# Kernel tuning notes

Measured on AMD Instinct MI355X. Metric: run time of the kernel, lower is better.

The kernel has to match this reference:

```python
import jax, jax.numpy as jnp
import numpy as np

B_SZ, L, H, P = 16, 1024, 256, 256
DT_MIN, DT_MAX = 1e-3, 1e-1


def setup_inputs() -> dict:
    key = jax.random.key(0)
    ks = jax.random.split(key, 6)
    u = jax.random.normal(ks[0], (B_SZ, L, H), dtype=jnp.float32)
    # Stable diagonal init (stands in for HiPPO-LegS diag: negative real part,
    # spread imaginary parts) so exp(Lambda*Delta) has |.|<1 over long scans.
    Lambda_re = -0.5 * jnp.ones((P,), jnp.float32)
    Lambda_im = jnp.pi * jnp.arange(P, dtype=jnp.float32)
    Bp = jax.random.normal(ks[1], (P, H, 2), jnp.float32) / jnp.sqrt(2.0 * H)  # (P,H,2) real/imag
    Cp = jax.random.normal(ks[2], (H, P, 2), jnp.float32) / jnp.sqrt(2.0 * P)  # (H,P,2) real/imag
    D = jax.random.normal(ks[3], (H,), jnp.float32)
    log_step = (jax.random.uniform(ks[4], (P, 1), jnp.float32)
                * (jnp.log(DT_MAX) - jnp.log(DT_MIN)) + jnp.log(DT_MIN))
    return {"u": u, "Lambda_re": Lambda_re, "Lambda_im": Lambda_im,
            "B": Bp, "C": Cp, "D": D, "log_step": log_step}


def _binop(ei, ej):
    # S5 associative scan element: (A, Bu); compose linear recurrences.
    ai, bi = ei
    aj, bj = ej
    return aj * ai, aj * bi + bj


def reference(u, Lambda_re, Lambda_im, B, C, D, log_step):
    # clip_eigs=False, step_rescale=1.0, conj_sym=True, discretization='zoh'
    Lambda = Lambda_re + 1j * Lambda_im                     # (P,) complex
    B_tilde = B[..., 0] + 1j * B[..., 1]                    # (P,H) complex
    C_tilde = C[..., 0] + 1j * C[..., 1]                    # (H,P) complex
    Delta = jnp.exp(log_step[:, 0])                         # (P,)
    # ZOH discretization
    Lambda_bar = jnp.exp(Lambda * Delta)                    # (P,)
    B_bar = ((Lambda_bar - 1.0) / Lambda)[:, None] * B_tilde  # (P,H)
    # Input projection: (B, L, P) complex
    Bu = jnp.einsum('ph,blh->blp', B_bar, u.astype(B_bar.dtype))
    Lam = jnp.broadcast_to(Lambda_bar, Bu.shape)            # (B, L, P)
    # Parallel associative scan over time axis
    _, xs = jax.lax.associative_scan(_binop, (Lam, Bu), axis=1)  # states (B,L,P)
    # Output projection; conj_sym -> 2 * real part
    ys = 2.0 * jnp.einsum('hp,blp->blh', C_tilde, xs).real  # (B,L,H)
    return ys + D * u                                       # feedthrough
```

## Files before the change

### kernel.cpp

```cpp
#include <hip/hip_runtime.h>
#include <hip/hip_bf16.h>
#include <math.h>

#define BB     16
#define LSEQ   1024
#define HH     256
#define PP     256
#define MROWS  (BB*LSEQ)
#define LC     32
#define NC     (LSEQ/LC)
#define NCHUNK (BB*NC)

#define OFF_W1T  0u
#define OFF_W2T  262144u
#define OFF_CEND 524288u
#define OFF_CPRE 1572864u
#define OFF_XS   2621440u

typedef __attribute__((ext_vector_type(8))) short short8;
typedef __attribute__((ext_vector_type(4))) float floatx4;

__device__ __forceinline__ float bf2f(unsigned hs) {
    union { unsigned u; float f; } v; v.u = hs << 16; return v.f;
}
__device__ __forceinline__ unsigned short f2bs(float f) {
    __hip_bfloat16 h = __float2bfloat16(f);
    union { __hip_bfloat16 h; unsigned short s; } v; v.h = h; return v.s;
}
__device__ __forceinline__ unsigned packbf(float r, float i) {
    return (unsigned)f2bs(r) | ((unsigned)f2bs(i) << 16);
}
__device__ __forceinline__ void async16(const void* g, void* l) {
    __builtin_amdgcn_global_load_lds(
        (const __attribute__((address_space(1))) unsigned*)g,
        (__attribute__((address_space(3))) unsigned*)l, 16, 0, 0);
}
__device__ __forceinline__ float2 lam_pow(float lr, float li, float dtt) {
    float m = expf(lr * dtt);
    return make_float2(m * cosf(li * dtt), m * sinf(li * dtt));
}

__global__ void k_prep(const float* __restrict__ Bm, const float* __restrict__ Cm,
                       const float* __restrict__ Lr, const float* __restrict__ Li,
                       const float* __restrict__ ls, char* __restrict__ ws) {
    int blk = blockIdx.x, t = threadIdx.x;
    if (blk < 256) {
        int p = blk, h = t;
        float lr = Lr[p], li = Li[p];
        float dt = expf(ls[p]);
        float2 lam = lam_pow(lr, li, dt);
        float den = lr * lr + li * li;
        float nr = lam.x - 1.0f, ni = lam.y;
        float cr = (nr * lr + ni * li) / den;
        float ci = (ni * lr - nr * li) / den;
        float br = Bm[(p * HH + h) * 2 + 0];
        float bi = Bm[(p * HH + h) * 2 + 1];
        unsigned short* w1 = (unsigned short*)(ws + OFF_W1T);
        w1[(2 * p) * 256 + h]     = f2bs(cr * br - ci * bi);
        w1[(2 * p + 1) * 256 + h] = f2bs(cr * bi + ci * br);
    } else {
        int h = blk - 256, p = t;
        float c_r = Cm[(h * PP + p) * 2 + 0];
        float c_i = Cm[(h * PP + p) * 2 + 1];
        ((unsigned*)(ws + OFF_W2T))[h * 256 + p] = packbf(2.0f * c_r, -2.0f * c_i);
    }
}

__global__ __launch_bounds__(256) void k_g1scan(
        const float* __restrict__ u, const float* __restrict__ Lr,
        const float* __restrict__ Li, const float* __restrict__ ls,
        char* __restrict__ ws) {
    __shared__ char smem[2048 + 32768];
    unsigned short* As = (unsigned short*)smem;
    char* Bs = smem + 2048;
    const unsigned short* W = (const unsigned short*)(ws + OFF_W1T);
    const int tid = threadIdx.x;
    const int wave = tid >> 6, lane = tid & 63;
    const int q = lane >> 4, rr = lane & 15;
    const int c4 = lane & 3, r4 = lane >> 2;
    const int bc = blockIdx.x;
    const int m0 = bc * LC;

    floatx4 acc[2][8];
    #pragma unroll
    for (int i = 0; i < 2; ++i)
        #pragma unroll
        for (int j = 0; j < 8; ++j) acc[i][j] = (floatx4)0.0f;

    const int urow = tid >> 3, ucol4 = (tid & 7) * 4;
    for (int k0 = 0; k0 < 256; k0 += 32) {
        __syncthreads();
        float4 v = *(const float4*)(u + (size_t)(m0 + urow) * 256 + k0 + ucol4);
        *(uint2*)((char*)As + urow * 64 + ucol4 * 2) =
            make_uint2(packbf(v.x, v.y), packbf(v.z, v.w));
        #pragma unroll
        for (int t = wave; t < 32; t += 4)
            async16(W + (size_t)(t * 16 + r4) * 256 + k0 + c4 * 8,
                    Bs + t * 1024 + lane * 16);
        __syncthreads();
        short8 a0 = *(const short8*)((char*)As + rr * 64 + q * 16);
        short8 a1 = *(const short8*)((char*)As + (16 + rr) * 64 + q * 16);
        #pragma unroll
        for (int j = 0; j < 8; ++j) {
            short8 b = *(const short8*)(Bs + ((wave * 8 + j) * 16 + rr) * 64 + q * 16);
            acc[0][j] = __builtin_amdgcn_mfma_f32_16x16x32_bf16(a0, b, acc[0][j], 0, 0, 0);
            acc[1][j] = __builtin_amdgcn_mfma_f32_16x16x32_bf16(a1, b, acc[1][j], 0, 0, 0);
        }
    }

    __syncthreads();
    unsigned short* X = (unsigned short*)Bs;
    #pragma unroll
    for (int i = 0; i < 2; ++i)
        #pragma unroll
        for (int j = 0; j < 8; ++j)
            #pragma unroll
            for (int r0 = 0; r0 < 4; ++r0)
                X[(i * 16 + q * 4 + r0) * 512 + wave * 128 + j * 16 + rr] =
                    f2bs(acc[i][j][r0]);
    __syncthreads();

    int p = tid;
    float dt = expf(ls[p]);
    float2 lam = lam_pow(Lr[p], Li[p], dt);
    unsigned* X32 = (unsigned*)Bs;
    unsigned* xs32 = (unsigned*)(ws + OFF_XS);
    float xr = 0.0f, xi = 0.0f;
    for (int j = 0; j < LC; ++j) {
        unsigned cv = X32[j * 256 + p];
        float br = bf2f(cv & 0xffffu), bi = bf2f(cv >> 16);
        float nr = fmaf(lam.x, xr, fmaf(-lam.y, xi, br));
        float ni = fmaf(lam.x, xi, fmaf(lam.y, xr, bi));
        xr = nr; xi = ni;
        xs32[(size_t)(m0 + j) * 256 + p] = packbf(xr, xi);
    }
    ((float2*)(ws + OFF_CEND))[bc * 256 + p] = make_float2(xr, xi);
}

__global__ void k_scanB(const float* __restrict__ Lr, const float* __restrict__ Li,
                        const float* __restrict__ ls, char* __restrict__ ws) {
    int p = threadIdx.x, b = blockIdx.x;
    float dt = expf(ls[p]);
    float2 g = lam_pow(Lr[p], Li[p], dt * LC);
    float2* cend = (float2*)(ws + OFF_CEND);
    float2* cpre = (float2*)(ws + OFF_CPRE);
    float sr = 0.0f, si = 0.0f;
    for (int c = 0; c < NC; ++c) {
        int off = (b * NC + c) * 256 + p;
        cpre[off] = make_float2(sr, si);
        float2 e = cend[off];
        float nr = g.x * sr - g.y * si + e.x;
        float ni = g.x * si + g.y * sr + e.y;
        sr = nr; si = ni;
    }
}

__global__ void k_scanC(const float* __restrict__ Lr, const float* __restrict__ Li,
                        const float* __restrict__ ls, char* __restrict__ ws) {
    int p = threadIdx.x, bc = blockIdx.x;
    float dt = expf(ls[p]);
    float2 lam = lam_pow(Lr[p], Li[p], dt);
    float2 cr = ((const float2*)(ws + OFF_CPRE))[bc * 256 + p];
    float pr = lam.x, pi = lam.y;
    unsigned* xs32 = (unsigned*)(ws + OFF_XS);
    size_t idx = (size_t)bc * LC * 256 + p;
    for (int j = 0; j < LC; ++j) {
        float ar = pr * cr.x - pi * cr.y;
        float ai = pr * cr.y + pi * cr.x;
        unsigned v = xs32[idx];
        xs32[idx] = packbf(bf2f(v & 0xffffu) + ar, bf2f(v >> 16) + ai);
        float nr = pr * lam.x - pi * lam.y;
        pi = pr * lam.y + pi * lam.x; pr = nr;
        idx += 256;
    }
}

__global__ __launch_bounds__(256) void k_gemm2(
        const char* __restrict__ ws_c, const float* __restrict__ D,
        const float* __restrict__ u, float* __restrict__ out) {
    __shared__ unsigned short As[128 * 32];
    __shared__ unsigned short Bs[128 * 32];
    const unsigned short* A = (const unsigned short*)(ws_c + OFF_XS);
    const unsigned short* W = (const unsigned short*)(ws_c + OFF_W2T);
    const int tid = threadIdx.x;
    const int wave = tid >> 6, lane = tid & 63;
    const int q = lane >> 4, rr = lane & 15;
    const int c4 = lane & 3, r4 = lane >> 2;
    const int wm = wave & 1, wn = wave >> 1;
    const int m0 = blockIdx.y * 128, n0 = blockIdx.x * 128;

    floatx4 acc[4][4];
    #pragma unroll
    for (int i = 0; i < 4; ++i)
        #pragma unroll
        for (int j = 0; j < 4; ++j) acc[i][j] = (floatx4)0.0f;

    for (int k0 = 0; k0 < 512; k0 += 32) {
        __syncthreads();
        #pragma unroll
        for (int t = wave; t < 8; t += 4)
            async16(A + (size_t)(m0 + t * 16 + r4) * 512 + k0 + c4 * 8,
                    (char*)As + t * 1024 + lane * 16);
        #pragma unroll
        for (int t = wave; t < 8; t += 4)
            async16(W + (size_t)(n0 + t * 16 + r4) * 512 + k0 + c4 * 8,
                    (char*)Bs + t * 1024 + lane * 16);
        __syncthreads();
        short8 a[4], b[4];
        #pragma unroll
        for (int i = 0; i < 4; ++i)
            a[i] = *(const short8*)((const char*)As + (wm * 64 + i * 16 + rr) * 64 + q * 16);
        #pragma unroll
        for (int j = 0; j < 4; ++j)
            b[j] = *(const short8*)((const char*)Bs + (wn * 64 + j * 16 + rr) * 64 + q * 16);
        #pragma unroll
        for (int i = 0; i < 4; ++i)
            #pragma unroll
            for (int j = 0; j < 4; ++j)
                acc[i][j] = __builtin_amdgcn_mfma_f32_16x16x32_bf16(a[i], b[j], acc[i][j], 0, 0, 0);
    }

    #pragma unroll
    for (int i = 0; i < 4; ++i) {
        int mbase = m0 + wm * 64 + i * 16 + q * 4;
        #pragma unroll
        for (int j = 0; j < 4; ++j) {
            int col = n0 + wn * 64 + j * 16 + rr;
            #pragma unroll
            for (int r0 = 0; r0 < 4; ++r0) {
                int row = mbase + r0;
                float v = acc[i][j][r0] + D[col] * u[(size_t)row * 256 + col];
                out[(size_t)row * 256 + col] = v;
            }
        }
    }
}

extern "C" void kernel_launch(void* const* d_in, const int* in_sizes, int n_in,
                              void* d_out, int out_size, void* d_ws, size_t ws_size,
                              hipStream_t stream) {
    const float* u  = (const float*)d_in[0];
    const float* Lr = (const float*)d_in[1];
    const float* Li = (const float*)d_in[2];
    const float* Bm = (const float*)d_in[3];
    const float* Cm = (const float*)d_in[4];
    const float* D  = (const float*)d_in[5];
    const float* ls = (const float*)d_in[6];
    float* out = (float*)d_out;
    char* ws = (char*)d_ws;

    k_prep<<<512, 256, 0, stream>>>(Bm, Cm, Lr, Li, ls, ws);
    k_g1scan<<<NCHUNK, 256, 0, stream>>>(u, Lr, Li, ls, ws);
    k_scanB<<<BB, 256, 0, stream>>>(Lr, Li, ls, ws);
    k_scanC<<<NCHUNK, 256, 0, stream>>>(Lr, Li, ls, ws);
    k_gemm2<<<dim3(2, MROWS / 128), 256, 0, stream>>>(ws, D, u, out);
}
```

Measured before the change: 123.4 us.

## Fuse prep, chunk scan, carry propagation and output GEMM into one cooperative kernel

Replaces five kernel launches with a single cooperative kernel that uses grid-wide syncs between the weight prep, the chunked input GEMM and scan, and the carry fix-up plus output GEMM. Each block keeps its 32-row chunk of scan states in padded shared memory, so the xs tensor never goes through global memory. Each block recomputes its own chunk carry prefix serially from the chunk-end states instead of running a separate scan kernel. In exchange it depends on all 512 blocks being co-resident, pays for grid barriers, and uses about 51 KB of LDS per block, which can lower occupancy.

```diff
diff --git a/kernel.cpp b/kernel.cpp
--- a/kernel.cpp
+++ b/kernel.cpp
@@ -1,12 +1,14 @@
 #include <hip/hip_runtime.h>
 #include <hip/hip_bf16.h>
+#include <hip/hip_cooperative_groups.h>
 #include <math.h>
+
+namespace cg = cooperative_groups;
 
 #define BB     16
 #define LSEQ   1024
 #define HH     256
 #define PP     256
-#define MROWS  (BB*LSEQ)
 #define LC     32
 #define NC     (LSEQ/LC)
 #define NCHUNK (BB*NC)
@@ -14,8 +16,8 @@
 #define OFF_W1T  0u
 #define OFF_W2T  262144u
 #define OFF_CEND 524288u
-#define OFF_CPRE 1572864u
-#define OFF_XS   2621440u
+
+#define XSTRIDE 520
 
 typedef __attribute__((ext_vector_type(8))) short short8;
 typedef __attribute__((ext_vector_type(4))) float floatx4;
@@ -40,62 +42,64 @@
     return make_float2(m * cosf(li * dtt), m * sinf(li * dtt));
 }
 
-__global__ void k_prep(const float* __restrict__ Bm, const float* __restrict__ Cm,
-                       const float* __restrict__ Lr, const float* __restrict__ Li,
-                       const float* __restrict__ ls, char* __restrict__ ws) {
-    int blk = blockIdx.x, t = threadIdx.x;
-    if (blk < 256) {
-        int p = blk, h = t;
-        float lr = Lr[p], li = Li[p];
-        float dt = expf(ls[p]);
-        float2 lam = lam_pow(lr, li, dt);
-        float den = lr * lr + li * li;
-        float nr = lam.x - 1.0f, ni = lam.y;
-        float cr = (nr * lr + ni * li) / den;
-        float ci = (ni * lr - nr * li) / den;
+__global__ __launch_bounds__(256, 2) void k_fused(
+        const float* __restrict__ u, const float* __restrict__ Lr,
+        const float* __restrict__ Li, const float* __restrict__ Bm,
+        const float* __restrict__ Cm, const float* __restrict__ D,
+        const float* __restrict__ ls, float* __restrict__ out,
+        char* __restrict__ ws) {
+    cg::grid_group grid = cg::this_grid();
+    __shared__ char smem[51712];
+    unsigned short* As = (unsigned short*)smem;
+    char*           Bs = smem + 2048;
+    unsigned short* X  = (unsigned short*)(smem + 2048);
+    unsigned*      X32 = (unsigned*)(smem + 2048);
+    char*          Bs2 = smem + 35328;
+
+    const int tid = threadIdx.x, bc = blockIdx.x;
+    const int wave = tid >> 6, lane = tid & 63;
+    const int q = lane >> 4, rr = lane & 15;
+    const int c4 = lane & 3, r4 = lane >> 2;
+
+    if (bc < 256) {
+        int p = bc, h = tid;
+        float lr0 = Lr[p], li0 = Li[p];
+        float dt0 = expf(ls[p]);
+        float2 lam0 = lam_pow(lr0, li0, dt0);
+        float den = lr0 * lr0 + li0 * li0;
+        float nr = lam0.x - 1.0f, ni = lam0.y;
+        float cr = (nr * lr0 + ni * li0) / den;
+        float ci = (ni * lr0 - nr * li0) / den;
         float br = Bm[(p * HH + h) * 2 + 0];
         float bi = Bm[(p * HH + h) * 2 + 1];
         unsigned short* w1 = (unsigned short*)(ws + OFF_W1T);
         w1[(2 * p) * 256 + h]     = f2bs(cr * br - ci * bi);
         w1[(2 * p + 1) * 256 + h] = f2bs(cr * bi + ci * br);
     } else {
-        int h = blk - 256, p = t;
+        int h = bc - 256, p = tid;
         float c_r = Cm[(h * PP + p) * 2 + 0];
         float c_i = Cm[(h * PP + p) * 2 + 1];
         ((unsigned*)(ws + OFF_W2T))[h * 256 + p] = packbf(2.0f * c_r, -2.0f * c_i);
     }
-}
-
-__global__ __launch_bounds__(256) void k_g1scan(
-        const float* __restrict__ u, const float* __restrict__ Lr,
-        const float* __restrict__ Li, const float* __restrict__ ls,
-        char* __restrict__ ws) {
-    __shared__ char smem[2048 + 32768];
-    unsigned short* As = (unsigned short*)smem;
-    char* Bs = smem + 2048;
-    const unsigned short* W = (const unsigned short*)(ws + OFF_W1T);
-    const int tid = threadIdx.x;
-    const int wave = tid >> 6, lane = tid & 63;
-    const int q = lane >> 4, rr = lane & 15;
-    const int c4 = lane & 3, r4 = lane >> 2;
-    const int bc = blockIdx.x;
+    grid.sync();
+
     const int m0 = bc * LC;
-
+    const unsigned short* W1 = (const unsigned short*)(ws + OFF_W1T);
     floatx4 acc[2][8];
     #pragma unroll
     for (int i = 0; i < 2; ++i)
         #pragma unroll
         for (int j = 0; j < 8; ++j) acc[i][j] = (floatx4)0.0f;
 
-    const int urow = tid >> 3, ucol4 = (tid & 7) * 4;
+    const int urow = tid >> 3, ucol = (tid & 7) * 4;
     for (int k0 = 0; k0 < 256; k0 += 32) {
         __syncthreads();
-        float4 v = *(const float4*)(u + (size_t)(m0 + urow) * 256 + k0 + ucol4);
-        *(uint2*)((char*)As + urow * 64 + ucol4 * 2) =
+        float4 v = *(const float4*)(u + (size_t)(m0 + urow) * 256 + k0 + ucol);
+        *(uint2*)((char*)As + urow * 64 + ucol * 2) =
             make_uint2(packbf(v.x, v.y), packbf(v.z, v.w));
         #pragma unroll
         for (int t = wave; t < 32; t += 4)
-            async16(W + (size_t)(t * 16 + r4) * 256 + k0 + c4 * 8,
+            async16(W1 + (size_t)(t * 16 + r4) * 256 + k0 + c4 * 8,
                     Bs + t * 1024 + lane * 16);
         __syncthreads();
         short8 a0 = *(const short8*)((char*)As + rr * 64 + q * 16);
@@ -107,130 +111,91 @@
             acc[1][j] = __builtin_amdgcn_mfma_f32_16x16x32_bf16(a1, b, acc[1][j], 0, 0, 0);
         }
     }
-
     __syncthreads();
-    unsigned short* X = (unsigned short*)Bs;
     #pragma unroll
     for (int i = 0; i < 2; ++i)
         #pragma unroll
         for (int j = 0; j < 8; ++j)
             #pragma unroll
             for (int r0 = 0; r0 < 4; ++r0)
-                X[(i * 16 + q * 4 + r0) * 512 + wave * 128 + j * 16 + rr] =
+                X[(i * 16 + q * 4 + r0) * XSTRIDE + wave * 128 + j * 16 + rr] =
                     f2bs(acc[i][j][r0]);
     __syncthreads();
 
-    int p = tid;
-    float dt = expf(ls[p]);
-    float2 lam = lam_pow(Lr[p], Li[p], dt);
-    unsigned* X32 = (unsigned*)Bs;
-    unsigned* xs32 = (unsigned*)(ws + OFF_XS);
+    const int p = tid;
+    const float lr = Lr[p], li = Li[p];
+    const float dt = expf(ls[p]);
+    const float2 lam = lam_pow(lr, li, dt);
     float xr = 0.0f, xi = 0.0f;
     for (int j = 0; j < LC; ++j) {
-        unsigned cv = X32[j * 256 + p];
+        unsigned cv = X32[j * (XSTRIDE / 2) + p];
         float br = bf2f(cv & 0xffffu), bi = bf2f(cv >> 16);
         float nr = fmaf(lam.x, xr, fmaf(-lam.y, xi, br));
         float ni = fmaf(lam.x, xi, fmaf(lam.y, xr, bi));
         xr = nr; xi = ni;
-        xs32[(size_t)(m0 + j) * 256 + p] = packbf(xr, xi);
+        X32[j * (XSTRIDE / 2) + p] = packbf(xr, xi);
     }
     ((float2*)(ws + OFF_CEND))[bc * 256 + p] = make_float2(xr, xi);
-}
-
-__global__ void k_scanB(const float* __restrict__ Lr, const float* __restrict__ Li,
-                        const float* __restrict__ ls, char* __restrict__ ws) {
-    int p = threadIdx.x, b = blockIdx.x;
-    float dt = expf(ls[p]);
-    float2 g = lam_pow(Lr[p], Li[p], dt * LC);
-    float2* cend = (float2*)(ws + OFF_CEND);
-    float2* cpre = (float2*)(ws + OFF_CPRE);
+
+    grid.sync();
+
+    const int b = bc >> 5, c = bc & (NC - 1);
+    const float2 g = lam_pow(lr, li, dt * (float)LC);
+    const float2* cend = (const float2*)(ws + OFF_CEND);
     float sr = 0.0f, si = 0.0f;
-    for (int c = 0; c < NC; ++c) {
-        int off = (b * NC + c) * 256 + p;
-        cpre[off] = make_float2(sr, si);
-        float2 e = cend[off];
+    for (int cc = 0; cc < c; ++cc) {
+        float2 e = cend[(b * NC + cc) * 256 + p];
         float nr = g.x * sr - g.y * si + e.x;
         float ni = g.x * si + g.y * sr + e.y;
         sr = nr; si = ni;
     }
-}
-
-__global__ void k_scanC(const float* __restrict__ Lr, const float* __restrict__ Li,
-                        const float* __restrict__ ls, char* __restrict__ ws) {
-    int p = threadIdx.x, bc = blockIdx.x;
-    float dt = expf(ls[p]);
-    float2 lam = lam_pow(Lr[p], Li[p], dt);
-    float2 cr = ((const float2*)(ws + OFF_CPRE))[bc * 256 + p];
+
     float pr = lam.x, pi = lam.y;
-    unsigned* xs32 = (unsigned*)(ws + OFF_XS);
-    size_t idx = (size_t)bc * LC * 256 + p;
     for (int j = 0; j < LC; ++j) {
-        float ar = pr * cr.x - pi * cr.y;
-        float ai = pr * cr.y + pi * cr.x;
-        unsigned v = xs32[idx];
-        xs32[idx] = packbf(bf2f(v & 0xffffu) + ar, bf2f(v >> 16) + ai);
+        float ar = pr * sr - pi * si;
+        float ai = pr * si + pi * sr;
+        unsigned v = X32[j * (XSTRIDE / 2) + p];
+        X32[j * (XSTRIDE / 2) + p] = packbf(bf2f(v & 0xffffu) + ar,
+                                            bf2f(v >> 16) + ai);
         float nr = pr * lam.x - pi * lam.y;
         pi = pr * lam.y + pi * lam.x; pr = nr;
-        idx += 256;
-    }
-}
-
-__global__ __launch_bounds__(256) void k_gemm2(
-        const char* __restrict__ ws_c, const float* __restrict__ D,
-        const float* __restrict__ u, float* __restrict__ out) {
-    __shared__ unsigned short As[128 * 32];
-    __shared__ unsigned short Bs[128 * 32];
-    const unsigned short* A = (const unsigned short*)(ws_c + OFF_XS);
-    const unsigned short* W = (const unsigned short*)(ws_c + OFF_W2T);
-    const int tid = threadIdx.x;
-    const int wave = tid >> 6, lane = tid & 63;
-    const int q = lane >> 4, rr = lane & 15;
-    const int c4 = lane & 3, r4 = lane >> 2;
-    const int wm = wave & 1, wn = wave >> 1;
-    const int m0 = blockIdx.y * 128, n0 = blockIdx.x * 128;
-
-    floatx4 acc[4][4];
-    #pragma unroll
-    for (int i = 0; i < 4; ++i)
-        #pragma unroll
-        for (int j = 0; j < 4; ++j) acc[i][j] = (floatx4)0.0f;
+    }
+    __syncthreads();
+
+    const unsigned short* W2 = (const unsigned short*)(ws + OFF_W2T);
+    floatx4 acc2[2][4];
+    #pragma unroll
+    for (int i = 0; i < 2; ++i)
+        #pragma unroll
+        for (int j = 0; j < 4; ++j) acc2[i][j] = (floatx4)0.0f;
 
     for (int k0 = 0; k0 < 512; k0 += 32) {
         __syncthreads();
         #pragma unroll
-        for (int t = wave; t < 8; t += 4)
-            async16(A + (size_t)(m0 + t * 16 + r4) * 512 + k0 + c4 * 8,
-                    (char*)As + t * 1024 + lane * 16);
-        #pragma unroll
-        for (int t = wave; t < 8; t += 4)
-            async16(W + (size_t)(n0 + t * 16 + r4) * 512 + k0 + c4 * 8,
-                    (char*)Bs + t * 1024 + lane * 16);
-        __syncthreads();
-        short8 a[4], b[4];
-        #pragma unroll
-        for (int i = 0; i < 4; ++i)
-            a[i] = *(const short8*)((const char*)As + (wm * 64 + i * 16 + rr) * 64 + q * 16);
-        #pragma unroll
-        for (int j = 0; j < 4; ++j)
-            b[j] = *(const short8*)((const char*)Bs + (wn * 64 + j * 16 + rr) * 64 + q * 16);
-        #pragma unroll
-        for (int i = 0; i < 4; ++i)
-            #pragma unroll
-            for (int j = 0; j < 4; ++j)
-                acc[i][j] = __builtin_amdgcn_mfma_f32_16x16x32_bf16(a[i], b[j], acc[i][j], 0, 0, 0);
-    }
-
-    #pragma unroll
-    for (int i = 0; i < 4; ++i) {
-        int mbase = m0 + wm * 64 + i * 16 + q * 4;
+        for (int t = wave; t < 16; t += 4)
+            async16(W2 + (size_t)(t * 16 + r4) * 512 + k0 + c4 * 8,
+                    Bs2 + t * 1024 + lane * 16);
+        __syncthreads();
+        short8 a0 = *(const short8*)((char*)X + rr * (XSTRIDE * 2) + k0 * 2 + q * 16);
+        short8 a1 = *(const short8*)((char*)X + (16 + rr) * (XSTRIDE * 2) + k0 * 2 + q * 16);
         #pragma unroll
         for (int j = 0; j < 4; ++j) {
-            int col = n0 + wn * 64 + j * 16 + rr;
+            short8 bfr = *(const short8*)(Bs2 + ((wave * 4 + j) * 16 + rr) * 64 + q * 16);
+            acc2[0][j] = __builtin_amdgcn_mfma_f32_16x16x32_bf16(a0, bfr, acc2[0][j], 0, 0, 0);
+            acc2[1][j] = __builtin_amdgcn_mfma_f32_16x16x32_bf16(a1, bfr, acc2[1][j], 0, 0, 0);
+        }
+    }
+
+    #pragma unroll
+    for (int i = 0; i < 2; ++i) {
+        #pragma unroll
+        for (int j = 0; j < 4; ++j) {
+            int col = wave * 64 + j * 16 + rr;
             #pragma unroll
             for (int r0 = 0; r0 < 4; ++r0) {
-                int row = mbase + r0;
-                float v = acc[i][j][r0] + D[col] * u[(size_t)row * 256 + col];
-                out[(size_t)row * 256 + col] = v;
+                int row = m0 + i * 16 + q * 4 + r0;
+                size_t gi = (size_t)row * 256 + col;
+                out[gi] = acc2[i][j][r0] + D[col] * u[gi];
             }
         }
     }
@@ -249,9 +214,8 @@
     float* out = (float*)d_out;
     char* ws = (char*)d_ws;
 
-    k_prep<<<512, 256, 0, stream>>>(Bm, Cm, Lr, Li, ls, ws);
-    k_g1scan<<<NCHUNK, 256, 0, stream>>>(u, Lr, Li, ls, ws);
-    k_scanB<<<BB, 256, 0, stream>>>(Lr, Li, ls, ws);
-    k_scanC<<<NCHUNK, 256, 0, stream>>>(Lr, Li, ls, ws);
-    k_gemm2<<<dim3(2, MROWS / 128), 256, 0, stream>>>(ws, D, u, out);
-}
+    void* args[] = {(void*)&u, (void*)&Lr, (void*)&Li, (void*)&Bm, (void*)&Cm,
+                    (void*)&D, (void*)&ls, (void*)&out, (void*)&ws};
+    hipLaunchCooperativeKernel((const void*)k_fused, dim3(NCHUNK), dim3(256),
+                               args, 0, stream);
+}
```

Measured after the change: 229.7 us. 1.86x slower.

## Fuse chunk-carry scan into fixup kernel, widen g1scan blocks, shrink gemm2 tiles

Applied to the files above, without the earlier changes.

Replaces the serial per-batch carry scan (16 blocks) and the separate fixup kernel with a single kernel in which each chunk block recomputes its own incoming carry from earlier chunk ends. This removes a launch and the low-parallelism serial stage, at the cost of redundant work that grows quadratically with chunk index. The first GEMM+scan kernel now uses 512 threads, with only half of them running the scan, and pads its LDS row stride to reduce bank conflicts. The output GEMM uses 64x64 tiles so more blocks are launched for better occupancy.

```diff
diff --git a/kernel.cpp b/kernel.cpp
--- a/kernel.cpp
+++ b/kernel.cpp
@@ -14,8 +14,9 @@
 #define OFF_W1T  0u
 #define OFF_W2T  262144u
 #define OFF_CEND 524288u
-#define OFF_CPRE 1572864u
-#define OFF_XS   2621440u
+#define OFF_XS   1572864u
+
+#define XSTRIDE 520
 
 typedef __attribute__((ext_vector_type(8))) short short8;
 typedef __attribute__((ext_vector_type(4))) float floatx4;
@@ -66,107 +67,101 @@
     }
 }
 
-__global__ __launch_bounds__(256) void k_g1scan(
+__global__ __launch_bounds__(512, 4) void k_g1scan(
         const float* __restrict__ u, const float* __restrict__ Lr,
         const float* __restrict__ Li, const float* __restrict__ ls,
         char* __restrict__ ws) {
-    __shared__ char smem[2048 + 32768];
-    unsigned short* As = (unsigned short*)smem;
-    char* Bs = smem + 2048;
-    const unsigned short* W = (const unsigned short*)(ws + OFF_W1T);
-    const int tid = threadIdx.x;
+    __shared__ char smem[2048 + 33280];
+    unsigned*  As32 = (unsigned*)smem;
+    char*      Bs   = smem + 2048;
+    unsigned short* X = (unsigned short*)(smem + 2048);
+    unsigned*  X32  = (unsigned*)(smem + 2048);
+    const unsigned short* W1 = (const unsigned short*)(ws + OFF_W1T);
+    const int tid = threadIdx.x, bc = blockIdx.x;
     const int wave = tid >> 6, lane = tid & 63;
     const int q = lane >> 4, rr = lane & 15;
     const int c4 = lane & 3, r4 = lane >> 2;
-    const int bc = blockIdx.x;
     const int m0 = bc * LC;
 
-    floatx4 acc[2][8];
+    floatx4 acc[2][4];
     #pragma unroll
     for (int i = 0; i < 2; ++i)
         #pragma unroll
-        for (int j = 0; j < 8; ++j) acc[i][j] = (floatx4)0.0f;
-
-    const int urow = tid >> 3, ucol4 = (tid & 7) * 4;
+        for (int j = 0; j < 4; ++j) acc[i][j] = (floatx4)0.0f;
+
+    const int urow = tid >> 4, ucol2 = (tid & 15) * 2;
     for (int k0 = 0; k0 < 256; k0 += 32) {
         __syncthreads();
-        float4 v = *(const float4*)(u + (size_t)(m0 + urow) * 256 + k0 + ucol4);
-        *(uint2*)((char*)As + urow * 64 + ucol4 * 2) =
-            make_uint2(packbf(v.x, v.y), packbf(v.z, v.w));
-        #pragma unroll
-        for (int t = wave; t < 32; t += 4)
-            async16(W + (size_t)(t * 16 + r4) * 256 + k0 + c4 * 8,
+        float2 v = *(const float2*)(u + (size_t)(m0 + urow) * 256 + k0 + ucol2);
+        As32[urow * 16 + (tid & 15)] = packbf(v.x, v.y);
+        #pragma unroll
+        for (int t = wave; t < 32; t += 8)
+            async16(W1 + (size_t)(t * 16 + r4) * 256 + k0 + c4 * 8,
                     Bs + t * 1024 + lane * 16);
         __syncthreads();
-        short8 a0 = *(const short8*)((char*)As + rr * 64 + q * 16);
-        short8 a1 = *(const short8*)((char*)As + (16 + rr) * 64 + q * 16);
-        #pragma unroll
-        for (int j = 0; j < 8; ++j) {
-            short8 b = *(const short8*)(Bs + ((wave * 8 + j) * 16 + rr) * 64 + q * 16);
+        short8 a0 = *(const short8*)((char*)As32 + rr * 64 + q * 16);
+        short8 a1 = *(const short8*)((char*)As32 + (16 + rr) * 64 + q * 16);
+        #pragma unroll
+        for (int j = 0; j < 4; ++j) {
+            short8 b = *(const short8*)(Bs + ((wave * 4 + j) * 16 + rr) * 64 + q * 16);
             acc[0][j] = __builtin_amdgcn_mfma_f32_16x16x32_bf16(a0, b, acc[0][j], 0, 0, 0);
             acc[1][j] = __builtin_amdgcn_mfma_f32_16x16x32_bf16(a1, b, acc[1][j], 0, 0, 0);
         }
     }
-
     __syncthreads();
-    unsigned short* X = (unsigned short*)Bs;
     #pragma unroll
     for (int i = 0; i < 2; ++i)
         #pragma unroll
-        for (int j = 0; j < 8; ++j)
+        for (int j = 0; j < 4; ++j)
             #pragma unroll
             for (int r0 = 0; r0 < 4; ++r0)
-                X[(i * 16 + q * 4 + r0) * 512 + wave * 128 + j * 16 + rr] =
+                X[(i * 16 + q * 4 + r0) * XSTRIDE + wave * 64 + j * 16 + rr] =
                     f2bs(acc[i][j][r0]);
     __syncthreads();
 
-    int p = tid;
-    float dt = expf(ls[p]);
-    float2 lam = lam_pow(Lr[p], Li[p], dt);
-    unsigned* X32 = (unsigned*)Bs;
-    unsigned* xs32 = (unsigned*)(ws + OFF_XS);
-    float xr = 0.0f, xi = 0.0f;
-    for (int j = 0; j < LC; ++j) {
-        unsigned cv = X32[j * 256 + p];
-        float br = bf2f(cv & 0xffffu), bi = bf2f(cv >> 16);
-        float nr = fmaf(lam.x, xr, fmaf(-lam.y, xi, br));
-        float ni = fmaf(lam.x, xi, fmaf(lam.y, xr, bi));
-        xr = nr; xi = ni;
-        xs32[(size_t)(m0 + j) * 256 + p] = packbf(xr, xi);
-    }
-    ((float2*)(ws + OFF_CEND))[bc * 256 + p] = make_float2(xr, xi);
-}
-
-__global__ void k_scanB(const float* __restrict__ Lr, const float* __restrict__ Li,
-                        const float* __restrict__ ls, char* __restrict__ ws) {
-    int p = threadIdx.x, b = blockIdx.x;
-    float dt = expf(ls[p]);
-    float2 g = lam_pow(Lr[p], Li[p], dt * LC);
-    float2* cend = (float2*)(ws + OFF_CEND);
-    float2* cpre = (float2*)(ws + OFF_CPRE);
+    if (tid < 256) {
+        const int p = tid;
+        const float2 lam = lam_pow(Lr[p], Li[p], expf(ls[p]));
+        unsigned* xs32 = (unsigned*)(ws + OFF_XS);
+        float xr = 0.0f, xi = 0.0f;
+        for (int j = 0; j < LC; ++j) {
+            unsigned cv = X32[j * (XSTRIDE / 2) + p];
+            float br = bf2f(cv & 0xffffu), bi = bf2f(cv >> 16);
+            float nr = fmaf(lam.x, xr, fmaf(-lam.y, xi, br));
+            float ni = fmaf(lam.x, xi, fmaf(lam.y, xr, bi));
+            xr = nr; xi = ni;
+            xs32[(size_t)(m0 + j) * 256 + p] = packbf(xr, xi);
+        }
+        ((float2*)(ws + OFF_CEND))[bc * 256 + p] = make_float2(xr, xi);
+    }
+}
+
+__global__ __launch_bounds__(256) void k_scanBC(
+        const float* __restrict__ Lr, const float* __restrict__ Li,
+        const float* __restrict__ ls, char* __restrict__ ws) {
+    const int p = threadIdx.x, bc = blockIdx.x;
+    const int b = bc >> 5, c = bc & (NC - 1);
+    if (c == 0) return;
+    const float dt = expf(ls[p]);
+    const float lr = Lr[p], li = Li[p];
+    const float2 lam = lam_pow(lr, li, dt);
+    const float2 g = lam_pow(lr, li, dt * (float)LC);
+    const float2* cend = (const float2*)(ws + OFF_CEND);
+
     float sr = 0.0f, si = 0.0f;
-    for (int c = 0; c < NC; ++c) {
-        int off = (b * NC + c) * 256 + p;
-        cpre[off] = make_float2(sr, si);
-        float2 e = cend[off];
-        float nr = g.x * sr - g.y * si + e.x;
-        float ni = g.x * si + g.y * sr + e.y;
+    for (int cc = 0; cc < c; ++cc) {
+        float2 e = cend[(size_t)(b * NC + cc) * 256 + p];
+        float nr = fmaf(g.x, sr, fmaf(-g.y, si, e.x));
+        float ni = fmaf(g.x, si, fmaf(g.y, sr, e.y));
         sr = nr; si = ni;
     }
-}
-
-__global__ void k_scanC(const float* __restrict__ Lr, const float* __restrict__ Li,
-                        const float* __restrict__ ls, char* __restrict__ ws) {
-    int p = threadIdx.x, bc = blockIdx.x;
-    float dt = expf(ls[p]);
-    float2 lam = lam_pow(Lr[p], Li[p], dt);
-    float2 cr = ((const float2*)(ws + OFF_CPRE))[bc * 256 + p];
+
     float pr = lam.x, pi = lam.y;
     unsigned* xs32 = (unsigned*)(ws + OFF_XS);
     size_t idx = (size_t)bc * LC * 256 + p;
     for (int j = 0; j < LC; ++j) {
-        float ar = pr * cr.x - pi * cr.y;
-        float ai = pr * cr.y + pi * cr.x;
+        float ar = pr * sr - pi * si;
+        float ai = pr * si + pi * sr;
         unsigned v = xs32[idx];
         xs32[idx] = packbf(bf2f(v & 0xffffu) + ar, bf2f(v >> 16) + ai);
         float nr = pr * lam.x - pi * lam.y;
@@ -175,11 +170,11 @@
     }
 }
 
-__global__ __launch_bounds__(256) void k_gemm2(
+__global__ __launch_bounds__(256, 4) void k_gemm2(
         const char* __restrict__ ws_c, const float* __restrict__ D,
         const float* __restrict__ u, float* __restrict__ out) {
-    __shared__ unsigned short As[128 * 32];
-    __shared__ unsigned short Bs[128 * 32];
+    __shared__ unsigned short As[64 * 32];
+    __shared__ unsigned short Bs[64 * 32];
     const unsigned short* A = (const unsigned short*)(ws_c + OFF_XS);
     const unsigned short* W = (const unsigned short*)(ws_c + OFF_W2T);
     const int tid = threadIdx.x;
@@ -187,50 +182,46 @@
     const int q = lane >> 4, rr = lane & 15;
     const int c4 = lane & 3, r4 = lane >> 2;
     const int wm = wave & 1, wn = wave >> 1;
-    const int m0 = blockIdx.y * 128, n0 = blockIdx.x * 128;
-
-    floatx4 acc[4][4];
-    #pragma unroll
-    for (int i = 0; i < 4; ++i)
-        #pragma unroll
-        for (int j = 0; j < 4; ++j) acc[i][j] = (floatx4)0.0f;
+    const int m0 = blockIdx.y * 64, n0 = blockIdx.x * 64;
+
+    floatx4 acc[2][2];
+    #pragma unroll
+    for (int i = 0; i < 2; ++i)
+        #pragma unroll
+        for (int j = 0; j < 2; ++j) acc[i][j] = (floatx4)0.0f;
 
     for (int k0 = 0; k0 < 512; k0 += 32) {
         __syncthreads();
-        #pragma unroll
-        for (int t = wave; t < 8; t += 4)
-            async16(A + (size_t)(m0 + t * 16 + r4) * 512 + k0 + c4 * 8,
-                    (char*)As + t * 1024 + lane * 16);
-        #pragma unroll
-        for (int t = wave; t < 8; t += 4)
-            async16(W + (size_t)(n0 + t * 16 + r4) * 512 + k0 + c4 * 8,
-                    (char*)Bs + t * 1024 + lane * 16);
-        __syncthreads();
-        short8 a[4], b[4];
-        #pragma unroll
-        for (int i = 0; i < 4; ++i)
-            a[i] = *(const short8*)((const char*)As + (wm * 64 + i * 16 + rr) * 64 + q * 16);
-        #pragma unroll
-        for (int j = 0; j < 4; ++j)
-            b[j] = *(const short8*)((const char*)Bs + (wn * 64 + j * 16 + rr) * 64 + q * 16);
-        #pragma unroll
-        for (int i = 0; i < 4; ++i)
+        async16(A + (size_t)(m0 + wave * 16 + r4) * 512 + k0 + c4 * 8,
+                (char*)As + wave * 1024 + lane * 16);
+        async16(W + (size_t)(n0 + wave * 16 + r4) * 512 + k0 + c4 * 8,
+                (char*)Bs + wave * 1024 + lane * 16);
+        __syncthreads();
+        short8 a[2], b[2];
+        #pragma unroll
+        for (int i = 0; i < 2; ++i)
+            a[i] = *(const short8*)((const char*)As + ((wm * 2 + i) * 16 + rr) * 64 + q * 16);
+        #pragma unroll
+        for (int j = 0; j < 2; ++j)
+            b[j] = *(const short8*)((const char*)Bs + ((wn * 2 + j) * 16 + rr) * 64 + q * 16);
+        #pragma unroll
+        for (int i = 0; i < 2; ++i)
             #pragma unroll
-            for (int j = 0; j < 4; ++j)
+            for (int j = 0; j < 2; ++j)
                 acc[i][j] = __builtin_amdgcn_mfma_f32_16x16x32_bf16(a[i], b[j], acc[i][j], 0, 0, 0);
     }
 
     #pragma unroll
-    for (int i = 0; i < 4; ++i) {
-        int mbase = m0 + wm * 64 + i * 16 + q * 4;
-        #pragma unroll
-        for (int j = 0; j < 4; ++j) {
-            int col = n0 + wn * 64 + j * 16 + rr;
+    for (int i = 0; i < 2; ++i) {
+        int mbase = m0 + wm * 32 + i * 16 + q * 4;
+        #pragma unroll
+        for (int j = 0; j < 2; ++j) {
+            int col = n0 + wn * 32 + j * 16 + rr;
             #pragma unroll
             for (int r0 = 0; r0 < 4; ++r0) {
                 int row = mbase + r0;
-                float v = acc[i][j][r0] + D[col] * u[(size_t)row * 256 + col];
-                out[(size_t)row * 256 + col] = v;
+                size_t gi = (size_t)row * 256 + col;
+                out[gi] = acc[i][j][r0] + D[col] * u[gi];
             }
         }
     }
@@ -250,8 +241,7 @@
     char* ws = (char*)d_ws;
 
     k_prep<<<512, 256, 0, stream>>>(Bm, Cm, Lr, Li, ls, ws);
-    k_g1scan<<<NCHUNK, 256, 0, stream>>>(u, Lr, Li, ls, ws);
-    k_scanB<<<BB, 256, 0, stream>>>(Lr, Li, ls, ws);
-    k_scanC<<<NCHUNK, 256, 0, stream>>>(Lr, Li, ls, ws);
-    k_gemm2<<<dim3(2, MROWS / 128), 256, 0, stream>>>(ws, D, u, out);
-}
+    k_g1scan<<<NCHUNK, 512, 0, stream>>>(u, Lr, Li, ls, ws);
+    k_scanBC<<<NCHUNK, 256, 0, stream>>>(Lr, Li, ls, ws);
+    k_gemm2<<<dim3(4, MROWS / 64), 256, 0, stream>>>(ws, D, u, out);
+}
```

Result: no change. 122.7 us (-0.6%).
